# Optimization experiments

Measured on AMD Instinct MI355X. Metric: run time of the kernel, lower is better.

## Reference

```python
import jax, jax.numpy as jnp
import numpy as np

B_SZ, IN_DIM, N_NEURONS, N_LAYERS, N_OUTS = 65536, 4, 512, 8, 4


def setup_inputs() -> dict:
    key = jax.random.key(0)
    ks = jax.random.split(key, 5)
    glorot = lambda k, shape: jax.random.normal(k, shape, jnp.float32) * np.sqrt(2.0 / (shape[-2] + shape[-1]))
    inputs = jax.random.normal(ks[0], (B_SZ, IN_DIM), jnp.float32)
    # GaussianRFF projection matrix (fixed random Gaussian)
    B_rff = jax.random.normal(ks[1], (IN_DIM, N_NEURONS // 2), jnp.float32)
    Ws = glorot(ks[2], (N_LAYERS, N_NEURONS, N_NEURONS))
    bs = jnp.zeros((N_LAYERS, N_NEURONS), jnp.float32)
    alphas = jnp.zeros((N_LAYERS + 1,), jnp.float32)  # LAAF slopes, init 0
    Wf = glorot(ks[3], (N_NEURONS, N_OUTS))           # final mixer, no bias
    scale = jnp.ones((N_OUTS,), jnp.float32)          # Scaler, no bias
    return {"inputs": inputs, "B_rff": B_rff, "Ws": Ws, "bs": bs,
            "alphas": alphas, "Wf": Wf, "scale": scale}


def _mlp(x, B_rff, Ws, bs, alphas, Wf, scale):
    # Gaussian random Fourier feature embedding -> [B, n_neurons]
    z = x @ B_rff
    u = jnp.concatenate([jnp.sin(z), jnp.cos(z)], axis=-1)
    L = Ws.shape[0]
    def step(u, p):
        W, b, a = p
        # LAAF sine layer: sin(w0 * (1 + alpha) * (uW + b)), w0 = 1.0
        return jnp.sin((1.0 + a) * (u @ W + b)), None
    u, _ = jax.lax.scan(step, u, (Ws, bs, alphas[:L]))
    return (u @ Wf) * scale  # [B, 4] = (A1, A2, A3, phi)


def reference(inputs, B_rff, Ws, bs, alphas, Wf, scale):
    f = lambda x: _mlp(x, B_rff, Ws, bs, alphas, Wf, scale)
    def jvp_col(col):
        tang = jnp.zeros_like(inputs).at[:, col].set(1.0)
        return jax.jvp(f, (inputs,), (tang,))
    # input columns: 0=t, 1=z, 2=x, 3=y
    P, dPdz = jvp_col(1)
    _, dPdx = jvp_col(2)
    _, dPdy = jvp_col(3)
    A1_y, A1_z = dPdy[:, 0:1], dPdz[:, 0:1]
    A2_x, A2_z = dPdx[:, 1:2], dPdz[:, 1:2]
    A3_x, A3_y = dPdx[:, 2:3], dPdy[:, 2:3]
    phi_x, phi_y, phi_z = dPdx[:, 3:4], dPdy[:, 3:4], dPdz[:, 3:4]
    u = (A3_y - A2_z) + phi_x
    v = (A1_z - A3_x) + phi_y
    w = (A2_x - A1_y) + phi_z
    return jnp.concatenate([u, v, w], axis=1)
```

## Files before the change

### kernel.cpp

```cpp
#include <hip/hip_runtime.h>
#include <stdint.h>


#define B_SZ   65536
#define NN     512
#define NL     8
#define SPB    16
#define MROWS  64
#define NKS    32
#define NG2    (NL*NKS)
#define LDS_A  (MROWS*1024)
#define LDS_TOTAL (LDS_A + 1024)

typedef _Float16 f16x8  __attribute__((ext_vector_type(8)));
typedef float    f32x16 __attribute__((ext_vector_type(16)));

__device__ __forceinline__ uint16_t f2h_bits(float f) {
  union { _Float16 h; uint16_t u; } v; v.h = (_Float16)f; return v.u;
}
__device__ __forceinline__ float h2f(uint16_t b) {
  union { uint16_t u; _Float16 h; } v; v.u = b; return (float)v.h;
}

__global__ __launch_bounds__(512) void prep_weights(const float* __restrict__ Ws,
                                                    uint16_t* __restrict__ img) {
  const int g2 = blockIdx.x;
  const int l  = g2 >> 5, ks = g2 & 31;
  const float* src = Ws + ((size_t)l << 18);
  char* dst = (char*)img + ((size_t)g2 << 14);
  #pragma unroll
  for (int it = 0; it < 2; ++it) {
    const int fidx = threadIdx.x + it*512;
    const int ln  = fidx & 63, sub = fidx >> 6;
    const int n     = (sub >> 1)*64 + (sub & 1)*32 + (ln & 31);
    const int kbase = ks*16 + (ln >> 5)*8;
    uint16_t h[8];
    #pragma unroll
    for (int e = 0; e < 8; ++e)
      h[e] = f2h_bits(src[(size_t)(kbase + e)*512 + n]);
    uint4 pk;
    pk.x = (uint32_t)h[0] | ((uint32_t)h[1] << 16);
    pk.y = (uint32_t)h[2] | ((uint32_t)h[3] << 16);
    pk.z = (uint32_t)h[4] | ((uint32_t)h[5] << 16);
    pk.w = (uint32_t)h[6] | ((uint32_t)h[7] << 16);
    *(uint4*)(dst + (size_t)fidx*16) = pk;
  }
}

__global__ __launch_bounds__(512, 4) void pinn_fused(
    const float* __restrict__ inputs, const float* __restrict__ Brff,
    const float* __restrict__ bs, const float* __restrict__ alphas,
    const float* __restrict__ Wf, const float* __restrict__ scl,
    const uint16_t* __restrict__ wimg, float* __restrict__ out)
{
  extern __shared__ char smem[];

  const int tid  = threadIdx.x;
  const int lane = tid & 63;
  const int wv   = tid >> 6;
  const int l31  = lane & 31;
  const int kh   = lane >> 5;
  const int sbase = blockIdx.x * SPB;

  const char* wb = (const char*)wimg + ((size_t)(wv*2) << 10) + (size_t)lane*16;

  f16x8 bfA0 = *(const f16x8*)(wb);
  f16x8 bfA1 = *(const f16x8*)(wb + 1024);
  f16x8 bfB0 = *(const f16x8*)(wb + 16384);
  f16x8 bfB1 = *(const f16x8*)(wb + 16384 + 1024);

  {
    const int k = tid, col = k & 255;
    const bool iscos = (k >= 256);
    const float b0 = Brff[col];
    const float b1 = Brff[256 + col];
    const float b2 = Brff[512 + col];
    const float b3 = Brff[768 + col];
    const int koff = 2*k;
    for (int s = 0; s < SPB; ++s) {
      const float4 x = *(const float4*)(inputs + ((size_t)(sbase + s) << 2));
      const float z = x.x*b0 + x.y*b1 + x.z*b2 + x.w*b3;
      const float szn = __sinf(z), czn = __cosf(z);
      const float u0 = iscos ? czn : szn;
      const float dz = iscos ? -szn : czn;
      const int m0 = 4*s;
      *(uint16_t*)(smem + (size_t)(m0+0)*1024 + (koff ^ (((m0+0) & 7)*16))) = f2h_bits(u0);
      *(uint16_t*)(smem + (size_t)(m0+1)*1024 + (koff ^ (((m0+1) & 7)*16))) = f2h_bits(dz*b1);
      *(uint16_t*)(smem + (size_t)(m0+2)*1024 + (koff ^ (((m0+2) & 7)*16))) = f2h_bits(dz*b2);
      *(uint16_t*)(smem + (size_t)(m0+3)*1024 + (koff ^ (((m0+3) & 7)*16))) = f2h_bits(dz*b3);
    }
  }
  __syncthreads();

  const int rx   = (l31 & 7) * 16;
  const int hoff = kh * 16;
  char* arow0 = smem + (size_t)l31 * 1024;
  char* arow1 = arow0 + 32*1024;

  f16x8 afA0 = *(const f16x8*)(arow0 + (hoff ^ rx));
  f16x8 afA1 = *(const f16x8*)(arow1 + (hoff ^ rx));
  f16x8 afB0, afB1;

  const f32x16 zz = {0,0,0,0,0,0,0,0,0,0,0,0,0,0,0,0};

  for (int l = 0; l < NL; ++l) {
    f32x16 a00 = zz, a01 = zz, a10 = zz, a11 = zz;
    const int g2b = l*NKS;

    #pragma unroll 1
    for (int t = 0; t < NKS/2; ++t) {
      const int ks = 2*t;
      {
        const int co = ((ks + 1)*32 + hoff) ^ rx;
        afB0 = *(const f16x8*)(arow0 + co);
        afB1 = *(const f16x8*)(arow1 + co);
      }
      __builtin_amdgcn_s_setprio(1);
      a00 = __builtin_amdgcn_mfma_f32_32x32x16_f16(afA0, bfA0, a00, 0, 0, 0);
      a01 = __builtin_amdgcn_mfma_f32_32x32x16_f16(afA0, bfA1, a01, 0, 0, 0);
      a10 = __builtin_amdgcn_mfma_f32_32x32x16_f16(afA1, bfA0, a10, 0, 0, 0);
      a11 = __builtin_amdgcn_mfma_f32_32x32x16_f16(afA1, bfA1, a11, 0, 0, 0);
      __builtin_amdgcn_s_setprio(0);
      {
        const int gt = g2b + ks + 2;
        if (gt < NG2) {
          const char* p = wb + ((size_t)gt << 14);
          bfA0 = *(const f16x8*)(p);
          bfA1 = *(const f16x8*)(p + 1024);
        }
      }
      if (t + 1 < NKS/2) {
        const int co = ((ks + 2)*32 + hoff) ^ rx;
        afA0 = *(const f16x8*)(arow0 + co);
        afA1 = *(const f16x8*)(arow1 + co);
      }
      __builtin_amdgcn_s_setprio(1);
      a00 = __builtin_amdgcn_mfma_f32_32x32x16_f16(afB0, bfB0, a00, 0, 0, 0);
      a01 = __builtin_amdgcn_mfma_f32_32x32x16_f16(afB0, bfB1, a01, 0, 0, 0);
      a10 = __builtin_amdgcn_mfma_f32_32x32x16_f16(afB1, bfB0, a10, 0, 0, 0);
      a11 = __builtin_amdgcn_mfma_f32_32x32x16_f16(afB1, bfB1, a11, 0, 0, 0);
      __builtin_amdgcn_s_setprio(0);
      {
        const int gt = g2b + ks + 3;
        if (gt < NG2) {
          const char* p = wb + ((size_t)gt << 14);
          bfB0 = *(const f16x8*)(p);
          bfB1 = *(const f16x8*)(p + 1024);
        }
      }
    }
    __syncthreads();

    const float opa = 1.0f + alphas[l];
    #pragma unroll
    for (int Nt = 0; Nt < 2; ++Nt) {
      const int nc = wv*64 + Nt*32 + l31;
      const float bias = bs[l*NN + nc];
      #pragma unroll
      for (int Mt = 0; Mt < 2; ++Mt) {
        const f32x16 c = (Mt == 0) ? (Nt == 0 ? a00 : a01)
                                   : (Nt == 0 ? a10 : a11);
        #pragma unroll
        for (int j = 0; j < 4; ++j) {
          const float hh = opa * (c[4*j] + bias);
          const float un = __sinf(hh);
          const float fc = opa * __cosf(hh);
          const float vv[4] = { un, fc*c[4*j+1], fc*c[4*j+2], fc*c[4*j+3] };
          const int m0 = Mt*32 + 8*j + 4*kh;
          #pragma unroll
          for (int s = 0; s < 4; ++s) {
            const int m = m0 + s;
            *(uint16_t*)(smem + (size_t)m*1024 + ((2*nc) ^ ((m & 7)*16))) = f2h_bits(vv[s]);
          }
        }
      }
    }
    __syncthreads();

    if (l + 1 < NL) {
      afA0 = *(const f16x8*)(arow0 + (hoff ^ rx));
      afA1 = *(const f16x8*)(arow1 + (hoff ^ rx));
    }
  }

  float* dp = (float*)(smem + LDS_A);
  const float4 sc4 = *(const float4*)scl;
  for (int rr = 0; rr < MROWS/8; ++rr) {
    const int m = wv*(MROWS/8) + rr;
    float p0 = 0.f, p1 = 0.f, p2 = 0.f, p3 = 0.f;
    #pragma unroll
    for (int j = 0; j < 8; ++j) {
      const int k = lane + j*64;
      float a = h2f(*(const uint16_t*)(smem + (size_t)m*1024 + ((2*k) ^ ((m & 7)*16))));
      float4 wf = ((const float4*)Wf)[k];
      p0 += a*wf.x; p1 += a*wf.y; p2 += a*wf.z; p3 += a*wf.w;
    }
    #pragma unroll
    for (int d = 1; d < 64; d <<= 1) {
      p0 += __shfl_xor(p0, d, 64);
      p1 += __shfl_xor(p1, d, 64);
      p2 += __shfl_xor(p2, d, 64);
      p3 += __shfl_xor(p3, d, 64);
    }
    if (lane == 0) {
      float4* o = (float4*)(dp + m*4);
      *o = make_float4(p0*sc4.x, p1*sc4.y, p2*sc4.z, p3*sc4.w);
    }
  }
  __syncthreads();

  if (tid < SPB*3) {
    const int sl = tid / 3, c = tid - sl*3;
    const float* d1 = dp + (sl*4 + 1)*4;
    const float* d2 = dp + (sl*4 + 2)*4;
    const float* d3 = dp + (sl*4 + 3)*4;
    float val;
    if (c == 0)      val = d3[2] - d1[1] + d2[3];
    else if (c == 1) val = d1[0] - d2[2] + d3[3];
    else             val = d2[1] - d3[0] + d1[3];
    out[(size_t)(sbase + sl)*3 + c] = val;
  }
}

extern "C" void kernel_launch(void* const* d_in, const int* in_sizes, int n_in,
                              void* d_out, int out_size, void* d_ws, size_t ws_size,
                              hipStream_t stream) {
  const float* inputs = (const float*)d_in[0];
  const float* Brff   = (const float*)d_in[1];
  const float* Ws     = (const float*)d_in[2];
  const float* bsp    = (const float*)d_in[3];
  const float* alph   = (const float*)d_in[4];
  const float* Wfp    = (const float*)d_in[5];
  const float* sclp   = (const float*)d_in[6];
  uint16_t* wimg = (uint16_t*)d_ws;

  prep_weights<<<NG2, 512, 0, stream>>>(Ws, wimg);
  const int nblocks = B_SZ / SPB;
  pinn_fused<<<nblocks, 512, LDS_TOTAL, stream>>>(inputs, Brff, bsp, alph, Wfp, sclp,
                                                  wimg, (float*)d_out);
}
```

Baseline: 1.343 ms.

## Retile LDS activation layout into MFMA-fragment blocks and fully unroll K loop

Changes the shared-memory activation layout from row-major 1KB rows with an XOR swizzle to K-tile-major blocks, so each MFMA A-fragment load is a contiguous 16-byte read with a new XOR pattern meant to avoid bank conflicts. The K loop is fully unrolled with macros, and the guarded weight prefetch becomes a clamped unconditional load, which removes branches. The aim is fewer LDS bank conflicts and less address arithmetic in the inner loop. In exchange, the epilogue's 2-byte scattered stores use a different conflict pattern, and full unrolling raises register pressure under the 512x4 launch bounds.

```diff
diff --git a/kernel.cpp b/kernel.cpp
--- a/kernel.cpp
+++ b/kernel.cpp
@@ -20,6 +20,12 @@
 }
 __device__ __forceinline__ float h2f(uint16_t b) {
   union { uint16_t u; _Float16 h; } v; v.u = b; return (float)v.h;
+}
+
+__device__ __forceinline__ int abyte(int m, int k) {
+  const int tile = k >> 4, khp = (k >> 3) & 1, e = k & 7;
+  const int mp = m ^ (khp << 2) ^ ((tile & 1) << 1);
+  return (tile << 11) + (khp << 10) + (mp << 4) + (e << 1);
 }
 
 __global__ __launch_bounds__(512) void prep_weights(const float* __restrict__ Ws,
@@ -62,12 +68,17 @@
   const int kh   = lane >> 5;
   const int sbase = blockIdx.x * SPB;
 
-  const char* wb = (const char*)wimg + ((size_t)(wv*2) << 10) + (size_t)lane*16;
-
-  f16x8 bfA0 = *(const f16x8*)(wb);
-  f16x8 bfA1 = *(const f16x8*)(wb + 1024);
-  f16x8 bfB0 = *(const f16x8*)(wb + 16384);
-  f16x8 bfB1 = *(const f16x8*)(wb + 16384 + 1024);
+  const char* wp  = (const char*)wimg;
+  const int  boff = wv*2048 + lane*16;
+
+  const int av0 = (kh << 10) + ((l31 ^ (kh << 2)) << 4);
+  const int av1 = av0 ^ 32;
+
+  f16x8 bA0, bA1, bB0, bB1;
+  bA0 = *(const f16x8*)(wp + boff);
+  bA1 = *(const f16x8*)(wp + boff + 1024);
+  bB0 = *(const f16x8*)(wp + 16384 + boff);
+  bB1 = *(const f16x8*)(wp + 16384 + boff + 1024);
 
   {
     const int k = tid, col = k & 255;
@@ -76,7 +87,8 @@
     const float b1 = Brff[256 + col];
     const float b2 = Brff[512 + col];
     const float b3 = Brff[768 + col];
-    const int koff = 2*k;
+    const int cb  = ((k >> 4) << 11) + (((k >> 3) & 1) << 10) + ((k & 7) << 1);
+    const int xm  = (((k >> 3) & 1) << 2) ^ (((k >> 4) & 1) << 1);
     for (int s = 0; s < SPB; ++s) {
       const float4 x = *(const float4*)(inputs + ((size_t)(sbase + s) << 2));
       const float z = x.x*b0 + x.y*b1 + x.z*b2 + x.w*b3;
@@ -84,70 +96,52 @@
       const float u0 = iscos ? czn : szn;
       const float dz = iscos ? -szn : czn;
       const int m0 = 4*s;
-      *(uint16_t*)(smem + (size_t)(m0+0)*1024 + (koff ^ (((m0+0) & 7)*16))) = f2h_bits(u0);
-      *(uint16_t*)(smem + (size_t)(m0+1)*1024 + (koff ^ (((m0+1) & 7)*16))) = f2h_bits(dz*b1);
-      *(uint16_t*)(smem + (size_t)(m0+2)*1024 + (koff ^ (((m0+2) & 7)*16))) = f2h_bits(dz*b2);
-      *(uint16_t*)(smem + (size_t)(m0+3)*1024 + (koff ^ (((m0+3) & 7)*16))) = f2h_bits(dz*b3);
+      *(uint16_t*)(smem + cb + (((m0+0) ^ xm) << 4)) = f2h_bits(u0);
+      *(uint16_t*)(smem + cb + (((m0+1) ^ xm) << 4)) = f2h_bits(dz*b1);
+      *(uint16_t*)(smem + cb + (((m0+2) ^ xm) << 4)) = f2h_bits(dz*b2);
+      *(uint16_t*)(smem + cb + (((m0+3) ^ xm) << 4)) = f2h_bits(dz*b3);
     }
   }
   __syncthreads();
 
-  const int rx   = (l31 & 7) * 16;
-  const int hoff = kh * 16;
-  char* arow0 = smem + (size_t)l31 * 1024;
-  char* arow1 = arow0 + 32*1024;
-
-  f16x8 afA0 = *(const f16x8*)(arow0 + (hoff ^ rx));
-  f16x8 afA1 = *(const f16x8*)(arow1 + (hoff ^ rx));
-  f16x8 afB0, afB1;
+  f16x8 aA0, aA1, aB0, aB1;
+  aA0 = *(const f16x8*)(smem + av0);
+  aA1 = *(const f16x8*)(smem + av0 + 512);
 
   const f32x16 zz = {0,0,0,0,0,0,0,0,0,0,0,0,0,0,0,0};
+
+#define LDA(d0, d1, kss) do {                                              \
+    const int _av = ((kss) & 1) ? av1 : av0;                               \
+    d0 = *(const f16x8*)(smem + _av + (kss)*2048);                         \
+    d1 = *(const f16x8*)(smem + _av + (kss)*2048 + 512);                   \
+  } while (0)
+#define LDB(d0, d1, gg) do {                                               \
+    int _g = (gg); if (_g > NG2-1) _g = NG2-1;                             \
+    const char* _p = wp + ((size_t)_g << 14) + boff;                       \
+    d0 = *(const f16x8*)_p;                                                \
+    d1 = *(const f16x8*)(_p + 1024);                                       \
+  } while (0)
+#define MFMAQ(x0, x1, y0, y1) do {                                         \
+    __builtin_amdgcn_s_setprio(1);                                         \
+    a00 = __builtin_amdgcn_mfma_f32_32x32x16_f16(x0, y0, a00, 0, 0, 0);    \
+    a01 = __builtin_amdgcn_mfma_f32_32x32x16_f16(x0, y1, a01, 0, 0, 0);    \
+    a10 = __builtin_amdgcn_mfma_f32_32x32x16_f16(x1, y0, a10, 0, 0, 0);    \
+    a11 = __builtin_amdgcn_mfma_f32_32x32x16_f16(x1, y1, a11, 0, 0, 0);    \
+    __builtin_amdgcn_s_setprio(0);                                         \
+  } while (0)
 
   for (int l = 0; l < NL; ++l) {
     f32x16 a00 = zz, a01 = zz, a10 = zz, a11 = zz;
     const int g2b = l*NKS;
 
-    #pragma unroll 1
-    for (int t = 0; t < NKS/2; ++t) {
-      const int ks = 2*t;
-      {
-        const int co = ((ks + 1)*32 + hoff) ^ rx;
-        afB0 = *(const f16x8*)(arow0 + co);
-        afB1 = *(const f16x8*)(arow1 + co);
-      }
-      __builtin_amdgcn_s_setprio(1);
-      a00 = __builtin_amdgcn_mfma_f32_32x32x16_f16(afA0, bfA0, a00, 0, 0, 0);
-      a01 = __builtin_amdgcn_mfma_f32_32x32x16_f16(afA0, bfA1, a01, 0, 0, 0);
-      a10 = __builtin_amdgcn_mfma_f32_32x32x16_f16(afA1, bfA0, a10, 0, 0, 0);
-      a11 = __builtin_amdgcn_mfma_f32_32x32x16_f16(afA1, bfA1, a11, 0, 0, 0);
-      __builtin_amdgcn_s_setprio(0);
-      {
-        const int gt = g2b + ks + 2;
-        if (gt < NG2) {
-          const char* p = wb + ((size_t)gt << 14);
-          bfA0 = *(const f16x8*)(p);
-          bfA1 = *(const f16x8*)(p + 1024);
-        }
-      }
-      if (t + 1 < NKS/2) {
-        const int co = ((ks + 2)*32 + hoff) ^ rx;
-        afA0 = *(const f16x8*)(arow0 + co);
-        afA1 = *(const f16x8*)(arow1 + co);
-      }
-      __builtin_amdgcn_s_setprio(1);
-      a00 = __builtin_amdgcn_mfma_f32_32x32x16_f16(afB0, bfB0, a00, 0, 0, 0);
-      a01 = __builtin_amdgcn_mfma_f32_32x32x16_f16(afB0, bfB1, a01, 0, 0, 0);
-      a10 = __builtin_amdgcn_mfma_f32_32x32x16_f16(afB1, bfB0, a10, 0, 0, 0);
-      a11 = __builtin_amdgcn_mfma_f32_32x32x16_f16(afB1, bfB1, a11, 0, 0, 0);
-      __builtin_amdgcn_s_setprio(0);
-      {
-        const int gt = g2b + ks + 3;
-        if (gt < NG2) {
-          const char* p = wb + ((size_t)gt << 14);
-          bfB0 = *(const f16x8*)(p);
-          bfB1 = *(const f16x8*)(p + 1024);
-        }
-      }
+    #pragma unroll
+    for (int ks = 0; ks < NKS; ks += 2) {
+      LDA(aB0, aB1, ks + 1);
+      MFMAQ(aA0, aA1, bA0, bA1);
+      LDB(bA0, bA1, g2b + ks + 2);
+      if (ks + 2 < NKS) LDA(aA0, aA1, ks + 2);
+      MFMAQ(aB0, aB1, bB0, bB1);
+      LDB(bB0, bB1, g2b + ks + 3);
     }
     __syncthreads();
 
@@ -155,6 +149,8 @@
     #pragma unroll
     for (int Nt = 0; Nt < 2; ++Nt) {
       const int nc = wv*64 + Nt*32 + l31;
+      const int cb = ((nc >> 4) << 11) + (((nc >> 3) & 1) << 10) + ((nc & 7) << 1);
+      const int xm = (((nc >> 3) & 1) << 2) ^ (((nc >> 4) & 1) << 1);
       const float bias = bs[l*NN + nc];
       #pragma unroll
       for (int Mt = 0; Mt < 2; ++Mt) {
@@ -170,7 +166,7 @@
           #pragma unroll
           for (int s = 0; s < 4; ++s) {
             const int m = m0 + s;
-            *(uint16_t*)(smem + (size_t)m*1024 + ((2*nc) ^ ((m & 7)*16))) = f2h_bits(vv[s]);
+            *(uint16_t*)(smem + cb + ((m ^ xm) << 4)) = f2h_bits(vv[s]);
           }
         }
       }
@@ -178,8 +174,8 @@
     __syncthreads();
 
     if (l + 1 < NL) {
-      afA0 = *(const f16x8*)(arow0 + (hoff ^ rx));
-      afA1 = *(const f16x8*)(arow1 + (hoff ^ rx));
+      aA0 = *(const f16x8*)(smem + av0);
+      aA1 = *(const f16x8*)(smem + av0 + 512);
     }
   }
 
@@ -191,7 +187,7 @@
     #pragma unroll
     for (int j = 0; j < 8; ++j) {
       const int k = lane + j*64;
-      float a = h2f(*(const uint16_t*)(smem + (size_t)m*1024 + ((2*k) ^ ((m & 7)*16))));
+      float a = h2f(*(const uint16_t*)(smem + abyte(m, k)));
       float4 wf = ((const float4*)Wf)[k];
       p0 += a*wf.x; p1 += a*wf.y; p2 += a*wf.z; p3 += a*wf.w;
     }
```

Result: slower. 1.519 ms (+13.1%).
